# Performance work log

Measured on AMD Instinct MI355X. Metric: run time of the kernel, lower is better.

The kernel has to match this reference:

```python
import jax, jax.numpy as jnp
import numpy as np

N_HEADS = 8

def setup_inputs() -> dict:
    key = jax.random.key(0)
    ks = jax.random.split(key, 5)
    d = 256
    B, N = 2, 4096
    scale = 1.0 / np.sqrt(d)
    return {
        "x_q": jax.random.normal(ks[0], (B, N, d), jnp.float32),
        "x_kv": jax.random.normal(ks[1], (B, N, d), jnp.float32),
        "Wq": jax.random.normal(ks[2], (d, d), jnp.float32) * scale,
        "bq": jnp.zeros((d,), jnp.float32),
        "Wk": jax.random.normal(ks[3], (d, d), jnp.float32) * scale,
        "bk": jnp.zeros((d,), jnp.float32),
        "Wv": jax.random.normal(ks[4], (d, d), jnp.float32) * scale,
        "bv": jnp.zeros((d,), jnp.float32),
    }


def reference(x_q, x_kv, Wq, bq, Wk, bk, Wv, bv):
    B, Nq, d = x_q.shape
    H = N_HEADS
    dh = d // H
    # linear projections (torch Linear: x @ W^T + b)
    q = x_q @ Wq.T + bq            # [B, Nq, d]
    k = x_kv @ Wk.T + bk           # [B, Nk, d]
    v = x_kv @ Wv.T + bv           # [B, Nk, d]
    # split heads -> [B, H, N, dh]
    q = q.reshape(B, Nq, H, dh).transpose(0, 2, 1, 3)
    k = k.reshape(B, -1, H, dh).transpose(0, 2, 1, 3)
    v = v.reshape(B, -1, H, dh).transpose(0, 2, 1, 3)
    # scores [B, H, Nq, Nk], softmax over keys
    scores = jnp.einsum('bhqd,bhkd->bhqk', q, k) / jnp.sqrt(jnp.asarray(dh, q.dtype))
    attn = jax.nn.softmax(scores, axis=-1)
    out = jnp.einsum('bhqk,bhkd->bhqd', attn, v)   # [B, H, Nq, dh]
    return out.transpose(0, 2, 1, 3).reshape(B, Nq, H * dh)
```

## Files before the change

### kernel.cpp

```cpp
#include <hip/hip_runtime.h>
#include <stdint.h>

#define BATCH 2
#define NSEQ 4096
#define DM 256
#define NHEAD 8
#define DH 32
#define SCALE 0.17677669529663687f

typedef unsigned short ushort_t;
typedef __attribute__((ext_vector_type(8))) short short8;
typedef __attribute__((ext_vector_type(4))) float float4v;

__device__ __forceinline__ ushort_t f2bf(float f) {
    union { float f; uint32_t i; } x; x.f = f;
    uint32_t i = x.i;
    i += ((i >> 16) & 1u) + 0x7fffu;
    return (ushort_t)(i >> 16);
}
__device__ __forceinline__ uint32_t rne16(float f) {
    const uint32_t i = __float_as_uint(f);
    return i + 0x7fffu + ((i >> 16) & 1u);
}
__device__ __forceinline__ uint32_t pkrne(float a, float b) {
    return __builtin_amdgcn_perm(rne16(b), rne16(a), 0x07060302u);
}

#define RST 264
__global__ __launch_bounds__(256) void proj_kernel(
    const float* __restrict__ x_q, const float* __restrict__ x_kv,
    const float* __restrict__ Wq, const float* __restrict__ bq,
    const float* __restrict__ Wk, const float* __restrict__ bk,
    const float* __restrict__ Wv, const float* __restrict__ bv,
    ushort_t* __restrict__ Qh, ushort_t* __restrict__ Kh,
    ushort_t* __restrict__ Vt)
{
    const int mat = blockIdx.y;
    const int n0  = blockIdx.x * 32;
    const float* x    = (mat == 0) ? x_q : x_kv;
    const float* W    = (mat == 0) ? Wq : (mat == 1) ? Wk : Wv;
    const float* bias = (mat == 0) ? bq : (mat == 1) ? bk : bv;

    __shared__ __align__(16) ushort_t xls[32 * RST];
    const int t = threadIdx.x;

    {
        const int r  = t >> 3;
        const int c0 = (t & 7) * 32;
        const float* src = x + (size_t)(n0 + r) * DM + c0;
        uint32_t d[16];
        #pragma unroll
        for (int i = 0; i < 8; i++) {
            float4 v = *(const float4*)(src + i * 4);
            d[i * 2]     = pkrne(v.x, v.y);
            d[i * 2 + 1] = pkrne(v.z, v.w);
        }
        uint32_t* dst = (uint32_t*)&xls[r * RST + c0];
        #pragma unroll
        for (int i = 0; i < 4; i++)
            *(uint4*)(dst + i * 4) = *(const uint4*)&d[i * 4];
    }
    __syncthreads();

    const int w    = t >> 6;
    const int l    = t & 63;
    const int lm   = l & 15;
    const int quad = l >> 4;
    const int j0   = w * 64;

    float4v acc[2][4];
    #pragma unroll
    for (int rt = 0; rt < 2; rt++)
        #pragma unroll
        for (int jt = 0; jt < 4; jt++)
            acc[rt][jt] = (float4v){0.f, 0.f, 0.f, 0.f};

    for (int kc = 0; kc < DM / 32; kc++) {
        short8 af[2];
        #pragma unroll
        for (int rt = 0; rt < 2; rt++)
            af[rt] = *(const short8*)&xls[(rt * 16 + lm) * RST + kc * 32 + quad * 8];
        #pragma unroll
        for (int jt = 0; jt < 4; jt++) {
            const float* wp = W + (size_t)(j0 + jt * 16 + lm) * DM + kc * 32 + quad * 8;
            float4 w0 = *(const float4*)wp;
            float4 w1 = *(const float4*)(wp + 4);
            uint32_t bd[4] = { pkrne(w0.x, w0.y), pkrne(w0.z, w0.w),
                               pkrne(w1.x, w1.y), pkrne(w1.z, w1.w) };
            short8 bf = *(const short8*)bd;
            acc[0][jt] = __builtin_amdgcn_mfma_f32_16x16x32_bf16(af[0], bf, acc[0][jt], 0, 0, 0);
            acc[1][jt] = __builtin_amdgcn_mfma_f32_16x16x32_bf16(af[1], bf, acc[1][jt], 0, 0, 0);
        }
    }

    #pragma unroll
    for (int jt = 0; jt < 4; jt++) {
        const int j  = j0 + jt * 16 + lm;
        const int h  = j >> 5, dd = j & 31;
        const float bj = bias[j];
        #pragma unroll
        for (int rt = 0; rt < 2; rt++) {
            const int n  = n0 + rt * 16 + quad * 4;
            const int b  = n >> 12;
            const int nn = n & (NSEQ - 1);
            const int bh = b * NHEAD + h;
            if (mat == 2) {
                union { ushort_t u[4]; uint2 v; } pk;
                #pragma unroll
                for (int r = 0; r < 4; r++) pk.u[r] = f2bf(acc[rt][jt][r] + bj);
                *(uint2*)&Vt[((size_t)bh * DH + dd) * NSEQ + nn] = pk.v;
            } else {
                ushort_t* dstp = (mat == 0 ? Qh : Kh);
                #pragma unroll
                for (int r = 0; r < 4; r++)
                    dstp[((size_t)bh * NSEQ + nn + r) * DH + dd] = f2bf(acc[rt][jt][r] + bj);
            }
        }
    }
}

#define PST 40
__global__ __launch_bounds__(256) void fattn_kernel(
    const ushort_t* __restrict__ Qh, const ushort_t* __restrict__ Kh,
    const ushort_t* __restrict__ Vt, float* __restrict__ out)
{
    const int w    = threadIdx.x >> 6;
    const int l    = threadIdx.x & 63;
    const int lm   = l & 15;
    const int quad = l >> 4;
    const int qb   = blockIdx.x & 31;
    const int bh   = blockIdx.x >> 5;
    const int b    = bh >> 3, h = bh & 7;
    const int q0   = qb * 128 + w * 32;

    __shared__ __align__(16) ushort_t Pl[4][32 * PST];
    ushort_t* P = &Pl[w][0];

    const ushort_t* Qb = Qh + (size_t)bh * NSEQ * DH;
    const ushort_t* Kb = Kh + (size_t)bh * NSEQ * DH;
    const ushort_t* Vb = Vt + (size_t)bh * DH * NSEQ;

    short8 qf[2];
    #pragma unroll
    for (int qt = 0; qt < 2; qt++)
        qf[qt] = *(const short8*)(Qb + (size_t)(q0 + qt * 16 + lm) * DH + quad * 8);

    float4v accO[2][2];
    float   Lacc[2] = {0.f, 0.f};
    #pragma unroll
    for (int qt = 0; qt < 2; qt++) {
        accO[qt][0] = (float4v){0.f, 0.f, 0.f, 0.f};
        accO[qt][1] = (float4v){0.f, 0.f, 0.f, 0.f};
    }
    const float4v zero = {0.f, 0.f, 0.f, 0.f};

#define KLD(k, off) (*(const short8*)(Kb + (size_t)((k) + (off) + lm) * DH + quad * 8))
#define VLD(k, half) (*(const short8*)(Vb + (size_t)((half) + lm) * NSEQ + (k) + quad * 8))

    short8 kf0 = KLD(0, 0), kf1 = KLD(0, 16);
    short8 vf0 = VLD(0, 0), vf1 = VLD(0, 16);

    for (int k0 = 0; k0 < NSEQ; k0 += 32) {
        const int kn = (k0 + 32) & (NSEQ - 1);
        short8 nk0 = KLD(kn, 0), nk1 = KLD(kn, 16);
        short8 nv0 = VLD(kn, 0), nv1 = VLD(kn, 16);

        #pragma unroll
        for (int qt = 0; qt < 2; qt++) {
            float4v s0 = __builtin_amdgcn_mfma_f32_16x16x32_bf16(kf0, qf[qt], zero, 0, 0, 0);
            float4v s1 = __builtin_amdgcn_mfma_f32_16x16x32_bf16(kf1, qf[qt], zero, 0, 0, 0);
            float p0[4], p1[4];
            #pragma unroll
            for (int r = 0; r < 4; r++) {
                p0[r] = __expf(s0[r] * SCALE);
                p1[r] = __expf(s1[r] * SCALE);
            }
            Lacc[qt] += (p0[0] + p0[1]) + (p0[2] + p0[3])
                      + (p1[0] + p1[1]) + (p1[2] + p1[3]);
            uint2 w0 = { pkrne(p0[0], p0[1]), pkrne(p0[2], p0[3]) };
            uint2 w1 = { pkrne(p1[0], p1[1]), pkrne(p1[2], p1[3]) };
            *(uint2*)&P[(qt * 16 + lm) * PST + quad * 4]      = w0;
            *(uint2*)&P[(qt * 16 + lm) * PST + 16 + quad * 4] = w1;
        }

        #pragma unroll
        for (int qt = 0; qt < 2; qt++) {
            short8 pf = *(const short8*)&P[(qt * 16 + lm) * PST + quad * 8];
            accO[qt][0] = __builtin_amdgcn_mfma_f32_16x16x32_bf16(pf, vf0, accO[qt][0], 0, 0, 0);
            accO[qt][1] = __builtin_amdgcn_mfma_f32_16x16x32_bf16(pf, vf1, accO[qt][1], 0, 0, 0);
        }

        kf0 = nk0; kf1 = nk1; vf0 = nv0; vf1 = nv1;
    }
#undef KLD
#undef VLD

    float Lred[2];
    #pragma unroll
    for (int qt = 0; qt < 2; qt++) {
        float v = Lacc[qt];
        v += __shfl_xor(v, 16);
        v += __shfl_xor(v, 32);
        Lred[qt] = v;
    }

    #pragma unroll
    for (int qt = 0; qt < 2; qt++)
        #pragma unroll
        for (int r = 0; r < 4; r++) {
            const float Lrow = __shfl(Lred[qt], quad * 4 + r);
            const float inv  = 1.0f / Lrow;
            const int q = q0 + qt * 16 + quad * 4 + r;
            float* orow = out + ((size_t)b * NSEQ + q) * DM + h * DH;
            orow[lm]      = accO[qt][0][r] * inv;
            orow[16 + lm] = accO[qt][1][r] * inv;
        }
}

extern "C" void kernel_launch(void* const* d_in, const int* in_sizes, int n_in,
                              void* d_out, int out_size, void* d_ws, size_t ws_size,
                              hipStream_t stream)
{
    const float* x_q  = (const float*)d_in[0];
    const float* x_kv = (const float*)d_in[1];
    const float* Wq   = (const float*)d_in[2];
    const float* bq   = (const float*)d_in[3];
    const float* Wk   = (const float*)d_in[4];
    const float* bk   = (const float*)d_in[5];
    const float* Wv   = (const float*)d_in[6];
    const float* bv   = (const float*)d_in[7];
    float* out = (float*)d_out;

    const size_t per = (size_t)BATCH * NHEAD * NSEQ * DH;
    ushort_t* Qh = (ushort_t*)d_ws;
    ushort_t* Kh = Qh + per;
    ushort_t* Vt = Kh + per;

    dim3 pgrid(BATCH * NSEQ / 32, 3);
    proj_kernel<<<pgrid, 256, 0, stream>>>(x_q, x_kv, Wq, bq, Wk, bk, Wv, bv,
                                           Qh, Kh, Vt);

    fattn_kernel<<<BATCH * NHEAD * 32, 256, 0, stream>>>(Qh, Kh, Vt, out);
}
```

Measured before the change: 192.4 us.

## Keep attention probabilities in registers via permuted V layout and MFMA row sums

The projection kernel now writes V transposed with the keys inside each 32-key block permuted. This makes the S-MFMA output register layout line up with the A operand of the PV MFMA, so the LDS round trip for P is removed. Softmax row sums come from an extra MFMA against a ones vector instead of scalar adds and shuffles. Q is pre-scaled by scale*log2(e) so the inner loop uses a raw exp2 with no multiply. The cost is one extra MFMA per query tile per step and a more intricate layout contract between the two kernels.

```diff
diff --git a/kernel.cpp b/kernel.cpp
--- a/kernel.cpp
+++ b/kernel.cpp
@@ -7,6 +7,14 @@
 #define NHEAD 8
 #define DH 32
 #define SCALE 0.17677669529663687f
+
+#if __has_builtin(__builtin_amdgcn_exp2f)
+#define EXP2W(x) __builtin_amdgcn_exp2f(x)
+#define QPRE (SCALE * 1.44269504088896340736f)
+#else
+#define EXP2W(x) __expf((x) * 0.69314718055994530942f)
+#define QPRE (SCALE * 1.44269504088896340736f)
+#endif
 
 typedef unsigned short ushort_t;
 typedef __attribute__((ext_vector_type(8))) short short8;
@@ -93,33 +101,37 @@
         }
     }
 
+    const int bb = n0 >> 12;
+    const int cn = n0 & (NSEQ - 1);
     #pragma unroll
     for (int jt = 0; jt < 4; jt++) {
         const int j  = j0 + jt * 16 + lm;
         const int h  = j >> 5, dd = j & 31;
+        const int bh = bb * NHEAD + h;
         const float bj = bias[j];
         #pragma unroll
         for (int rt = 0; rt < 2; rt++) {
-            const int n  = n0 + rt * 16 + quad * 4;
-            const int b  = n >> 12;
-            const int nn = n & (NSEQ - 1);
-            const int bh = b * NHEAD + h;
             if (mat == 2) {
                 union { ushort_t u[4]; uint2 v; } pk;
                 #pragma unroll
                 for (int r = 0; r < 4; r++) pk.u[r] = f2bf(acc[rt][jt][r] + bj);
-                *(uint2*)&Vt[((size_t)bh * DH + dd) * NSEQ + nn] = pk.v;
-            } else {
-                ushort_t* dstp = (mat == 0 ? Qh : Kh);
+                *(uint2*)&Vt[((size_t)bh * DH + dd) * NSEQ + cn + quad * 8 + rt * 4] = pk.v;
+            } else if (mat == 0) {
+                const int nn = cn + rt * 16 + quad * 4;
                 #pragma unroll
                 for (int r = 0; r < 4; r++)
-                    dstp[((size_t)bh * NSEQ + nn + r) * DH + dd] = f2bf(acc[rt][jt][r] + bj);
+                    Qh[((size_t)bh * NSEQ + nn + r) * DH + dd] =
+                        f2bf((acc[rt][jt][r] + bj) * QPRE);
+            } else {
+                const int nn = cn + rt * 16 + quad * 4;
+                #pragma unroll
+                for (int r = 0; r < 4; r++)
+                    Kh[((size_t)bh * NSEQ + nn + r) * DH + dd] = f2bf(acc[rt][jt][r] + bj);
             }
         }
     }
 }
 
-#define PST 40
 __global__ __launch_bounds__(256) void fattn_kernel(
     const ushort_t* __restrict__ Qh, const ushort_t* __restrict__ Kh,
     const ushort_t* __restrict__ Vt, float* __restrict__ out)
@@ -133,9 +145,6 @@
     const int b    = bh >> 3, h = bh & 7;
     const int q0   = qb * 128 + w * 32;
 
-    __shared__ __align__(16) ushort_t Pl[4][32 * PST];
-    ushort_t* P = &Pl[w][0];
-
     const ushort_t* Qb = Qh + (size_t)bh * NSEQ * DH;
     const ushort_t* Kb = Kh + (size_t)bh * NSEQ * DH;
     const ushort_t* Vb = Vt + (size_t)bh * DH * NSEQ;
@@ -145,12 +154,16 @@
     for (int qt = 0; qt < 2; qt++)
         qf[qt] = *(const short8*)(Qb + (size_t)(q0 + qt * 16 + lm) * DH + quad * 8);
 
-    float4v accO[2][2];
-    float   Lacc[2] = {0.f, 0.f};
+    short8 ones;
+    #pragma unroll
+    for (int i = 0; i < 8; i++) ones[i] = (short)0x3F80;
+
+    float4v accO[2][2], accL[2];
     #pragma unroll
     for (int qt = 0; qt < 2; qt++) {
         accO[qt][0] = (float4v){0.f, 0.f, 0.f, 0.f};
         accO[qt][1] = (float4v){0.f, 0.f, 0.f, 0.f};
+        accL[qt]    = (float4v){0.f, 0.f, 0.f, 0.f};
     }
     const float4v zero = {0.f, 0.f, 0.f, 0.f};
 
@@ -172,22 +185,15 @@
             float p0[4], p1[4];
             #pragma unroll
             for (int r = 0; r < 4; r++) {
-                p0[r] = __expf(s0[r] * SCALE);
-                p1[r] = __expf(s1[r] * SCALE);
+                p0[r] = EXP2W(s0[r]);
+                p1[r] = EXP2W(s1[r]);
             }
-            Lacc[qt] += (p0[0] + p0[1]) + (p0[2] + p0[3])
-                      + (p1[0] + p1[1]) + (p1[2] + p1[3]);
-            uint2 w0 = { pkrne(p0[0], p0[1]), pkrne(p0[2], p0[3]) };
-            uint2 w1 = { pkrne(p1[0], p1[1]), pkrne(p1[2], p1[3]) };
-            *(uint2*)&P[(qt * 16 + lm) * PST + quad * 4]      = w0;
-            *(uint2*)&P[(qt * 16 + lm) * PST + 16 + quad * 4] = w1;
-        }
-
-        #pragma unroll
-        for (int qt = 0; qt < 2; qt++) {
-            short8 pf = *(const short8*)&P[(qt * 16 + lm) * PST + quad * 8];
+            uint32_t pd[4] = { pkrne(p0[0], p0[1]), pkrne(p0[2], p0[3]),
+                               pkrne(p1[0], p1[1]), pkrne(p1[2], p1[3]) };
+            short8 pf = *(const short8*)pd;
             accO[qt][0] = __builtin_amdgcn_mfma_f32_16x16x32_bf16(pf, vf0, accO[qt][0], 0, 0, 0);
             accO[qt][1] = __builtin_amdgcn_mfma_f32_16x16x32_bf16(pf, vf1, accO[qt][1], 0, 0, 0);
+            accL[qt]    = __builtin_amdgcn_mfma_f32_16x16x32_bf16(pf, ones, accL[qt], 0, 0, 0);
         }
 
         kf0 = nk0; kf1 = nk1; vf0 = nv0; vf1 = nv1;
@@ -195,21 +201,11 @@
 #undef KLD
 #undef VLD
 
-    float Lred[2];
-    #pragma unroll
-    for (int qt = 0; qt < 2; qt++) {
-        float v = Lacc[qt];
-        v += __shfl_xor(v, 16);
-        v += __shfl_xor(v, 32);
-        Lred[qt] = v;
-    }
-
     #pragma unroll
     for (int qt = 0; qt < 2; qt++)
         #pragma unroll
         for (int r = 0; r < 4; r++) {
-            const float Lrow = __shfl(Lred[qt], quad * 4 + r);
-            const float inv  = 1.0f / Lrow;
+            const float inv = 1.0f / accL[qt][r];
             const int q = q0 + qt * 16 + quad * 4 + r;
             float* orow = out + ((size_t)b * NSEQ + q) * DM + h * DH;
             orow[lm]      = accO[qt][0][r] * inv;
```

Measured after the change: 190.1 us. Within noise of the previous version (-1.2%).
